# Kernel tuning notes

Measured on AMD Instinct MI355X. Metric: run time of the kernel, lower is better.

Reference implementation:

```python
import jax, jax.numpy as jnp
import numpy as np

NUM_PROJS = 7
BLOCK_SIZE = 256   # key block size
SAMPLE_SIZE = 256  # residual sampled keys


def _gray_perm(n):
    # AngularLSH._unit_hamming_distance_array: Gray-code bucket permutation
    a = np.array([0, 1], dtype=np.int32)
    for i in range(1, n):
        a = np.concatenate([a, a[::-1] + 2 ** i])
    return a

PERM = jnp.asarray(_gray_perm(NUM_PROJS))
ENC = jnp.asarray(2 ** np.arange(NUM_PROJS), dtype=jnp.int32)


def lsh_hash(x, proj_dir):
    # sign-bit angular LSH -> Gray-code bucket id, [B,H,N]
    bits = (jnp.einsum('bhnd,dr->bhnr', x, proj_dir) > 0).astype(jnp.int32)
    return PERM[(bits * ENC).sum(-1)]


def exact_attention(q, k, v, scale, bias=None):
    s = jnp.einsum('...qd,...kd->...qk', q, k) * scale
    if bias is not None:
        s = s + bias
    lse = jax.nn.logsumexp(s, axis=-1, keepdims=True)
    attn = jnp.einsum('...qk,...kd->...qd', jnp.exp(s - lse), v)
    return attn, lse


def add_self_attentions(a1, l1, a2, l2):
    # stable online-softmax combination of two attention partials
    c = jax.nn.sigmoid(l1 - l2)  # = exp(l1)/(exp(l1)+exp(l2))
    return c * a1 + (1.0 - c) * a2, jnp.logaddexp(l1, l2)


def gather_seq(x, idx):
    # x: [B,H,N,D], idx: [B,H,S] -> [B,H,S,D]
    return jnp.take_along_axis(x, idx[..., None], axis=2)


def hyper_attention(query, key, value, proj_dir, sampled_set):
    B, H, Nq, D = query.shape
    Nk = key.shape[2]
    scale = D ** -0.5
    # --- LSH bucket sort of queries and keys (stable, matches torch.sort stable=True) ---
    q_idx = jnp.argsort(lsh_hash(query, proj_dir), axis=2, stable=True)
    k_idx = jnp.argsort(lsh_hash(key, proj_dir), axis=2, stable=True)
    q_idx_inv = jnp.argsort(q_idx, axis=2, stable=True)
    q_s = gather_seq(query, q_idx)
    k_s = gather_seq(key, k_idx)
    v_s = gather_seq(value, k_idx)
    # --- block-diagonal attention over LSH-sorted blocks ---
    nb = Nk // BLOCK_SIZE          # 32 blocks
    qbs = Nq // nb                 # query block size (== 256 here)
    attn_b, lse_b = exact_attention(
        q_s.reshape(B, H, nb, qbs, D),
        k_s.reshape(B, H, nb, BLOCK_SIZE, D),
        v_s.reshape(B, H, nb, BLOCK_SIZE, D),
        scale)
    attn_b = attn_b.reshape(B, H, Nq, D)
    lse_b = lse_b.reshape(B, H, Nq, 1)
    # --- residual: uniformly sampled keys, importance weight Nk/SAMPLE_SIZE ---
    k_sub = gather_seq(k_s, sampled_set)
    v_sub = gather_seq(v_s, sampled_set)
    q_pos = jnp.arange(Nq) // qbs                    # [Nq] query block ids
    s_blk = sampled_set // BLOCK_SIZE                # [B,H,S] sampled key block ids
    overlap = q_pos[None, None, :, None] == s_blk[:, :, None, :]  # [B,H,Nq,S]
    bias = jnp.where(overlap, jnp.finfo(query.dtype).min, 0.0).astype(query.dtype)
    attn_r, lse_r = exact_attention(q_s, k_sub, v_sub, scale, bias)
    lse_r = lse_r + jnp.asarray(np.log(Nk / SAMPLE_SIZE), lse_r.dtype)
    # --- combine partials via online LSE, then unsort queries ---
    attn, lse = add_self_attentions(attn_b, lse_b, attn_r, lse_r)
    attn = gather_seq(attn, q_idx_inv)
    return attn


def setup_inputs() -> dict:
    key = jax.random.key(0)
    kq, kk, kv, kp, ks = jax.random.split(key, 5)
    B, H, N, D = 2, 16, 8192, 64
    return {
        'query': jax.random.normal(kq, (B, H, N, D), jnp.float32),
        'key': jax.random.normal(kk, (B, H, N, D), jnp.float32),
        'value': jax.random.normal(kv, (B, H, N, D), jnp.float32),
        'proj_dir': jax.random.normal(kp, (D, NUM_PROJS), jnp.float32),
        'sampled_set': jax.random.randint(ks, (B, H, SAMPLE_SIZE), 0, N),
    }


def reference(query, key, value, proj_dir, sampled_set):
    return hyper_attention(query, key, value, proj_dir, sampled_set)
```

## Files before the change

### kernel.cpp

```cpp
#include <hip/hip_runtime.h>

#define BHX   32
#define NSEQ  8192
#define NMASK 8191
#define DIM   64
#define NPROJ 7
#define NBUCK 128
#define NBLK  32
#define QBS   256
#define SSIZE 256
#define LOG32 3.4657359027997265f
#define KPAD  72

typedef unsigned short u16;
typedef unsigned int   u32;
typedef unsigned char  u8;
typedef __attribute__((ext_vector_type(8))) short bf16x8;
typedef __attribute__((ext_vector_type(4))) float f32x4;

union B8U { u32 u[4]; bf16x8 v; };

__device__ __forceinline__ u16 f2bf(float f){
    u32 u = __float_as_uint(f);
    u32 r = u + 0x7fffu + ((u >> 16) & 1u);
    return (u16)(r >> 16);
}
__device__ __forceinline__ u32 pk2(float a, float b){
    return (u32)f2bf(a) | ((u32)f2bf(b) << 16);
}
__device__ __forceinline__ f32x4 mfma16(bf16x8 a, bf16x8 b, f32x4 c){
    return __builtin_amdgcn_mfma_f32_16x16x32_bf16(a, b, c, 0, 0, 0);
}

__global__ __launch_bounds__(256) void hash_kernel(
    const float* __restrict__ qg, const float* __restrict__ kg,
    const float* __restrict__ projg,
    u8* __restrict__ bkt)
{
    const int slab = blockIdx.x, bh = blockIdx.y, tz = blockIdx.z;
    const float* __restrict__ x = tz ? kg : qg;
    u8* __restrict__ ob = bkt + ((size_t)tz * BHX + bh) * NSEQ;

    __shared__ float projs[NPROJ][DIM];
    const int t = threadIdx.x;
    if (t < 112) {
        #pragma unroll
        for (int u = 0; u < 4; u++) {
            int e = t * 4 + u;
            projs[e % NPROJ][e / NPROJ] = projg[e];
        }
    }
    __syncthreads();

    const size_t bhN = (size_t)bh * NSEQ;
    #pragma unroll
    for (int j = 0; j < 4; j++) {
        int n = slab * 1024 + j * 256 + t;
        const float4* row = (const float4*)(x + (bhN + n) * DIM);
        float dot[NPROJ];
        #pragma unroll
        for (int r = 0; r < NPROJ; r++) dot[r] = 0.0f;
        #pragma unroll
        for (int c = 0; c < 16; c++) {
            float4 w = row[c];
            float f[4] = {w.x, w.y, w.z, w.w};
            #pragma unroll
            for (int u = 0; u < 4; u++) {
                float xv = f[u];
                int d = c * 4 + u;
                #pragma unroll
                for (int r = 0; r < NPROJ; r++) dot[r] += xv * projs[r][d];
            }
        }
        int code = 0;
        #pragma unroll
        for (int r = 0; r < NPROJ; r++) code |= (dot[r] > 0.0f ? 1 : 0) << r;
        ob[n] = (u8)(code ^ (code >> 1));
    }
}

__global__ __launch_bounds__(256) void sort_kernel(
    const u8* __restrict__ bkt,
    u16* __restrict__ qidx, u16* __restrict__ kidx)
{
    const int bh = blockIdx.x, tz = blockIdx.y;
    const u8* __restrict__ ib = bkt + ((size_t)tz * BHX + bh) * NSEQ;
    u16* __restrict__ idx = (tz ? kidx : qidx) + (size_t)bh * NSEQ;

    __shared__ u8  lb[NSEQ];
    __shared__ u16 hist[NBUCK][258];
    __shared__ int base[NBUCK];
    __shared__ int tot[NBUCK];

    const int t = threadIdx.x;
    {
        const uint4* src = (const uint4*)ib;
        uint4* dst = (uint4*)lb;
        dst[t] = src[t];
        dst[256 + t] = src[256 + t];
    }
    u32* hz = (u32*)&hist[0][0];
    for (int z = t; z < (NBUCK * 258) / 2; z += 256) hz[z] = 0u;
    __syncthreads();

    #pragma unroll 4
    for (int i = 0; i < 32; i++) hist[lb[t * 32 + i]][t]++;
    __syncthreads();

    if (t < NBUCK) {
        u32 run = 0;
        for (int c = 0; c < 256; c++) {
            u32 v = hist[t][c];
            hist[t][c] = (u16)run;
            run += v;
        }
        tot[t] = (int)run;
    }
    __syncthreads();
    if (t == 0) {
        int run = 0;
        for (int b = 0; b < NBUCK; b++) { base[b] = run; run += tot[b]; }
    }
    __syncthreads();

    #pragma unroll 4
    for (int i = 0; i < 32; i++) {
        int n = t * 32 + i;
        int b = lb[n];
        int pos = base[b] + hist[b][t];
        hist[b][t]++;
        idx[pos] = (u16)n;
    }
}

__global__ __launch_bounds__(256, 2) void attn_mfma(
    const float* __restrict__ qg, const float* __restrict__ kg,
    const float* __restrict__ vg,
    const u16* __restrict__ qidx, const u16* __restrict__ kidx,
    const int* __restrict__ samp,
    float* __restrict__ outg)
{
    __shared__ u16  Ks[64 * KPAD];
    __shared__ u16  Vt[64 * KPAD];
    __shared__ u16  Ps[4 * 64 * KPAD];
    __shared__ float addv[64];

    const int qb = blockIdx.x, bh = blockIdx.y, t = threadIdx.x;
    const int w = t >> 6, lane = t & 63, c = lane & 15, g = lane >> 4;
    const size_t bhN = (size_t)bh * NSEQ;

    int qi[4];
    bf16x8 qf[4][2];
    #pragma unroll
    for (int qt = 0; qt < 4; qt++) {
        qi[qt] = ((int)qidx[bhN + qb * QBS + w * 64 + qt * 16 + c]) & NMASK;
        const float* qr = qg + (bhN + (size_t)qi[qt]) * DIM;
        #pragma unroll
        for (int dk = 0; dk < 2; dk++) {
            int d0 = dk * 32 + g * 8;
            float4 x = *(const float4*)(qr + d0);
            float4 y = *(const float4*)(qr + d0 + 4);
            B8U f;
            f.u[0] = pk2(x.x * 0.125f, x.y * 0.125f);
            f.u[1] = pk2(x.z * 0.125f, x.w * 0.125f);
            f.u[2] = pk2(y.x * 0.125f, y.y * 0.125f);
            f.u[3] = pk2(y.z * 0.125f, y.w * 0.125f);
            qf[qt][dk] = f.v;
        }
    }

    f32x4 O[4][4];
    #pragma unroll
    for (int dt = 0; dt < 4; dt++)
        #pragma unroll
        for (int qt = 0; qt < 4; qt++) O[dt][qt] = (f32x4)0.0f;
    float m[4] = {-1e30f, -1e30f, -1e30f, -1e30f};
    float l[4] = {0.0f, 0.0f, 0.0f, 0.0f};

    for (int cc = 0; cc < 8; cc++) {
        __syncthreads();
        {
            int s = t >> 2, seg = (t & 3) * 16;
            int grow; float add;
            if (cc < 4) {
                grow = ((int)kidx[bhN + qb * QBS + cc * 64 + s]) & NMASK;
                add  = 0.0f;
            } else {
                int sidx = samp[bh * SSIZE + (cc - 4) * 64 + s] & NMASK;
                grow = ((int)kidx[bhN + sidx]) & NMASK;
                add  = ((sidx >> 8) == qb) ? -1e30f : LOG32;
            }
            const float4* kr = (const float4*)(kg + (bhN + (size_t)grow) * DIM + seg);
            float4 a = kr[0], b = kr[1], e = kr[2], d = kr[3];
            u32* dst = (u32*)&Ks[s * KPAD + seg];
            dst[0] = pk2(a.x, a.y); dst[1] = pk2(a.z, a.w);
            dst[2] = pk2(b.x, b.y); dst[3] = pk2(b.z, b.w);
            dst[4] = pk2(e.x, e.y); dst[5] = pk2(e.z, e.w);
            dst[6] = pk2(d.x, d.y); dst[7] = pk2(d.z, d.w);
            const float4* vr = (const float4*)(vg + (bhN + (size_t)grow) * DIM + seg);
            float4 va = vr[0], vb = vr[1], vc = vr[2], vd = vr[3];
            float vv[16] = {va.x, va.y, va.z, va.w, vb.x, vb.y, vb.z, vb.w,
                            vc.x, vc.y, vc.z, vc.w, vd.x, vd.y, vd.z, vd.w};
            #pragma unroll
            for (int i = 0; i < 16; i++) Vt[(seg + i) * KPAD + s] = f2bf(vv[i]);
            if ((t & 3) == 0) addv[s] = add;
        }
        __syncthreads();

        f32x4 addn[4];
        #pragma unroll
        for (int kt = 0; kt < 4; kt++)
            addn[kt] = *(const f32x4*)&addv[kt * 16 + g * 4];

        bf16x8 ka[4][2];
        #pragma unroll
        for (int kt = 0; kt < 4; kt++)
            #pragma unroll
            for (int dk = 0; dk < 2; dk++)
                ka[kt][dk] = *(const bf16x8*)&Ks[(kt * 16 + c) * KPAD + dk * 32 + g * 8];

        #pragma unroll
        for (int qt = 0; qt < 4; qt++) {
            f32x4 S[4];
            #pragma unroll
            for (int kt = 0; kt < 4; kt++) {
                S[kt] = (f32x4)0.0f;
                S[kt] = mfma16(ka[kt][0], qf[qt][0], S[kt]);
                S[kt] = mfma16(ka[kt][1], qf[qt][1], S[kt]);
            }
            float cmax = -1e30f;
            #pragma unroll
            for (int kt = 0; kt < 4; kt++)
                #pragma unroll
                for (int r = 0; r < 4; r++)
                    cmax = fmaxf(cmax, S[kt][r] + addn[kt][r]);
            cmax = fmaxf(cmax, __shfl_xor(cmax, 16));
            cmax = fmaxf(cmax, __shfl_xor(cmax, 32));
            float mnew  = fmaxf(m[qt], cmax);
            float alpha = __expf(m[qt] - mnew);
            m[qt] = mnew;
            float lsum = 0.0f;
            u16* prow = &Ps[(size_t)(w * 64 + qt * 16 + c) * KPAD];
            #pragma unroll
            for (int kt = 0; kt < 4; kt++) {
                float p0 = __expf(S[kt][0] + addn[kt][0] - mnew);
                float p1 = __expf(S[kt][1] + addn[kt][1] - mnew);
                float p2 = __expf(S[kt][2] + addn[kt][2] - mnew);
                float p3 = __expf(S[kt][3] + addn[kt][3] - mnew);
                lsum += (p0 + p1) + (p2 + p3);
                u32* pw = (u32*)&prow[kt * 16 + g * 4];
                pw[0] = pk2(p0, p1);
                pw[1] = pk2(p2, p3);
            }
            lsum += __shfl_xor(lsum, 16);
            lsum += __shfl_xor(lsum, 32);
            l[qt] = l[qt] * alpha + lsum;
            #pragma unroll
            for (int dt = 0; dt < 4; dt++) O[dt][qt] *= alpha;
        }

        #pragma unroll
        for (int kk = 0; kk < 2; kk++) {
            bf16x8 vfr[4], pfr[4];
            #pragma unroll
            for (int dt = 0; dt < 4; dt++)
                vfr[dt] = *(const bf16x8*)&Vt[(dt * 16 + c) * KPAD + kk * 32 + g * 8];
            #pragma unroll
            for (int qt = 0; qt < 4; qt++)
                pfr[qt] = *(const bf16x8*)&Ps[(size_t)(w * 64 + qt * 16 + c) * KPAD + kk * 32 + g * 8];
            #pragma unroll
            for (int dt = 0; dt < 4; dt++)
                #pragma unroll
                for (int qt = 0; qt < 4; qt++)
                    O[dt][qt] = mfma16(vfr[dt], pfr[qt], O[dt][qt]);
        }
    }

    #pragma unroll
    for (int qt = 0; qt < 4; qt++) {
        float inv = 1.0f / fmaxf(l[qt], 1e-30f);
        float* orow = outg + (bhN + (size_t)qi[qt]) * DIM;
        #pragma unroll
        for (int dt = 0; dt < 4; dt++) {
            f32x4 o = O[dt][qt] * inv;
            *(f32x4*)(orow + dt * 16 + g * 4) = o;
        }
    }
}

extern "C" void kernel_launch(void* const* d_in, const int* in_sizes, int n_in,
                              void* d_out, int out_size, void* d_ws, size_t ws_size,
                              hipStream_t stream)
{
    const float* qg   = (const float*)d_in[0];
    const float* kg   = (const float*)d_in[1];
    const float* vg   = (const float*)d_in[2];
    const float* pg   = (const float*)d_in[3];
    const int*   samp = (const int*)d_in[4];
    float* outg = (float*)d_out;

    u16* qidx = (u16*)d_ws;
    u16* kidx = qidx + BHX * NSEQ;
    u8*  bkt  = (u8*)(kidx + BHX * NSEQ);

    hipLaunchKernelGGL(hash_kernel, dim3(8, BHX, 2), dim3(256), 0, stream,
                       qg, kg, pg, bkt);
    hipLaunchKernelGGL(sort_kernel, dim3(BHX, 2), dim3(256), 0, stream,
                       bkt, qidx, kidx);
    hipLaunchKernelGGL(attn_mfma, dim3(NBLK, BHX), dim3(256), 0, stream,
                       qg, kg, vg, qidx, kidx, samp, outg);
}
```

Before: 314.4 us.

## Use 512-thread attention blocks, split K/V staging, swizzle V transpose, vectorize hash

The attention kernel moves to 512 threads per block, with each wave owning 32 queries instead of 64. This lowers per-thread register use and raises the number of waves per CU. The K and V loads are split between the two halves of the block, and the transposed V tile uses an XOR swizzle to cut LDS bank conflicts. The additive mask is folded into S right after the MFMA. The hash kernel reads the projection vectors from LDS as float4. The risk is that the smaller per-wave work makes each V fragment reused across fewer query tiles.

```diff
diff --git a/kernel.cpp b/kernel.cpp
--- a/kernel.cpp
+++ b/kernel.cpp
@@ -62,14 +62,14 @@
         for (int r = 0; r < NPROJ; r++) dot[r] = 0.0f;
         #pragma unroll
         for (int c = 0; c < 16; c++) {
-            float4 w = row[c];
-            float f[4] = {w.x, w.y, w.z, w.w};
-            #pragma unroll
-            for (int u = 0; u < 4; u++) {
-                float xv = f[u];
-                int d = c * 4 + u;
-                #pragma unroll
-                for (int r = 0; r < NPROJ; r++) dot[r] += xv * projs[r][d];
+            float4 wv = row[c];
+            #pragma unroll
+            for (int r = 0; r < NPROJ; r++) {
+                float4 p = *(const float4*)&projs[r][c * 4];
+                dot[r] += wv.x * p.x;
+                dot[r] += wv.y * p.y;
+                dot[r] += wv.z * p.z;
+                dot[r] += wv.w * p.w;
             }
         }
         int code = 0;
@@ -133,7 +133,7 @@
     }
 }
 
-__global__ __launch_bounds__(256, 2) void attn_mfma(
+__global__ __launch_bounds__(512, 4) void attn_mfma(
     const float* __restrict__ qg, const float* __restrict__ kg,
     const float* __restrict__ vg,
     const u16* __restrict__ qidx, const u16* __restrict__ kidx,
@@ -142,45 +142,47 @@
 {
     __shared__ u16  Ks[64 * KPAD];
     __shared__ u16  Vt[64 * KPAD];
-    __shared__ u16  Ps[4 * 64 * KPAD];
+    __shared__ u16  Ps[256 * KPAD];
     __shared__ float addv[64];
 
     const int qb = blockIdx.x, bh = blockIdx.y, t = threadIdx.x;
     const int w = t >> 6, lane = t & 63, c = lane & 15, g = lane >> 4;
     const size_t bhN = (size_t)bh * NSEQ;
 
-    int qi[4];
-    bf16x8 qf[4][2];
+    int qi[2];
+    bf16x8 qf[2][2];
     #pragma unroll
-    for (int qt = 0; qt < 4; qt++) {
-        qi[qt] = ((int)qidx[bhN + qb * QBS + w * 64 + qt * 16 + c]) & NMASK;
+    for (int qt = 0; qt < 2; qt++) {
+        qi[qt] = ((int)qidx[bhN + qb * QBS + w * 32 + qt * 16 + c]) & NMASK;
         const float* qr = qg + (bhN + (size_t)qi[qt]) * DIM;
         #pragma unroll
         for (int dk = 0; dk < 2; dk++) {
             int d0 = dk * 32 + g * 8;
-            float4 x = *(const float4*)(qr + d0);
-            float4 y = *(const float4*)(qr + d0 + 4);
+            float4 xx = *(const float4*)(qr + d0);
+            float4 yy = *(const float4*)(qr + d0 + 4);
             B8U f;
-            f.u[0] = pk2(x.x * 0.125f, x.y * 0.125f);
-            f.u[1] = pk2(x.z * 0.125f, x.w * 0.125f);
-            f.u[2] = pk2(y.x * 0.125f, y.y * 0.125f);
-            f.u[3] = pk2(y.z * 0.125f, y.w * 0.125f);
+            f.u[0] = pk2(xx.x * 0.125f, xx.y * 0.125f);
+            f.u[1] = pk2(xx.z * 0.125f, xx.w * 0.125f);
+            f.u[2] = pk2(yy.x * 0.125f, yy.y * 0.125f);
+            f.u[3] = pk2(yy.z * 0.125f, yy.w * 0.125f);
             qf[qt][dk] = f.v;
         }
     }
 
-    f32x4 O[4][4];
+    f32x4 O[4][2];
     #pragma unroll
     for (int dt = 0; dt < 4; dt++)
         #pragma unroll
-        for (int qt = 0; qt < 4; qt++) O[dt][qt] = (f32x4)0.0f;
-    float m[4] = {-1e30f, -1e30f, -1e30f, -1e30f};
-    float l[4] = {0.0f, 0.0f, 0.0f, 0.0f};
+        for (int qt = 0; qt < 2; qt++) O[dt][qt] = (f32x4)0.0f;
+    float m[2] = {-1e30f, -1e30f};
+    float l[2] = {0.0f, 0.0f};
 
     for (int cc = 0; cc < 8; cc++) {
         __syncthreads();
         {
-            int s = t >> 2, seg = (t & 3) * 16;
+            const int half = t >> 8;
+            const int tt = t & 255;
+            const int s = tt >> 2, seg = (tt & 3) * 16;
             int grow; float add;
             if (cc < 4) {
                 grow = ((int)kidx[bhN + qb * QBS + cc * 64 + s]) & NMASK;
@@ -190,27 +192,27 @@
                 grow = ((int)kidx[bhN + sidx]) & NMASK;
                 add  = ((sidx >> 8) == qb) ? -1e30f : LOG32;
             }
-            const float4* kr = (const float4*)(kg + (bhN + (size_t)grow) * DIM + seg);
-            float4 a = kr[0], b = kr[1], e = kr[2], d = kr[3];
-            u32* dst = (u32*)&Ks[s * KPAD + seg];
-            dst[0] = pk2(a.x, a.y); dst[1] = pk2(a.z, a.w);
-            dst[2] = pk2(b.x, b.y); dst[3] = pk2(b.z, b.w);
-            dst[4] = pk2(e.x, e.y); dst[5] = pk2(e.z, e.w);
-            dst[6] = pk2(d.x, d.y); dst[7] = pk2(d.z, d.w);
-            const float4* vr = (const float4*)(vg + (bhN + (size_t)grow) * DIM + seg);
-            float4 va = vr[0], vb = vr[1], vc = vr[2], vd = vr[3];
-            float vv[16] = {va.x, va.y, va.z, va.w, vb.x, vb.y, vb.z, vb.w,
-                            vc.x, vc.y, vc.z, vc.w, vd.x, vd.y, vd.z, vd.w};
-            #pragma unroll
-            for (int i = 0; i < 16; i++) Vt[(seg + i) * KPAD + s] = f2bf(vv[i]);
-            if ((t & 3) == 0) addv[s] = add;
+            if (half == 0) {
+                const float4* kr = (const float4*)(kg + (bhN + (size_t)grow) * DIM + seg);
+                float4 a = kr[0], b = kr[1], e = kr[2], d = kr[3];
+                u32* dst = (u32*)&Ks[s * KPAD + seg];
+                dst[0] = pk2(a.x, a.y); dst[1] = pk2(a.z, a.w);
+                dst[2] = pk2(b.x, b.y); dst[3] = pk2(b.z, b.w);
+                dst[4] = pk2(e.x, e.y); dst[5] = pk2(e.z, e.w);
+                dst[6] = pk2(d.x, d.y); dst[7] = pk2(d.z, d.w);
+                if ((tt & 3) == 0) addv[s] = add;
+            } else {
+                const float4* vr = (const float4*)(vg + (bhN + (size_t)grow) * DIM + seg);
+                float4 va = vr[0], vb = vr[1], ve = vr[2], vd = vr[3];
+                float vv[16] = {va.x, va.y, va.z, va.w, vb.x, vb.y, vb.z, vb.w,
+                                ve.x, ve.y, ve.z, ve.w, vd.x, vd.y, vd.z, vd.w};
+                const int col = (((s >> 3) ^ (tt & 3)) << 3) | (s & 7);
+                #pragma unroll
+                for (int i = 0; i < 16; i++)
+                    Vt[(seg + i) * KPAD + col] = f2bf(vv[i]);
+            }
         }
         __syncthreads();
-
-        f32x4 addn[4];
-        #pragma unroll
-        for (int kt = 0; kt < 4; kt++)
-            addn[kt] = *(const f32x4*)&addv[kt * 16 + g * 4];
 
         bf16x8 ka[4][2];
         #pragma unroll
@@ -220,33 +222,34 @@
                 ka[kt][dk] = *(const bf16x8*)&Ks[(kt * 16 + c) * KPAD + dk * 32 + g * 8];
 
         #pragma unroll
-        for (int qt = 0; qt < 4; qt++) {
+        for (int qt = 0; qt < 2; qt++) {
             f32x4 S[4];
             #pragma unroll
             for (int kt = 0; kt < 4; kt++) {
                 S[kt] = (f32x4)0.0f;
                 S[kt] = mfma16(ka[kt][0], qf[qt][0], S[kt]);
                 S[kt] = mfma16(ka[kt][1], qf[qt][1], S[kt]);
+                S[kt] += *(const f32x4*)&addv[kt * 16 + g * 4];
             }
             float cmax = -1e30f;
             #pragma unroll
             for (int kt = 0; kt < 4; kt++)
                 #pragma unroll
                 for (int r = 0; r < 4; r++)
-                    cmax = fmaxf(cmax, S[kt][r] + addn[kt][r]);
+                    cmax = fmaxf(cmax, S[kt][r]);
             cmax = fmaxf(cmax, __shfl_xor(cmax, 16));
             cmax = fmaxf(cmax, __shfl_xor(cmax, 32));
             float mnew  = fmaxf(m[qt], cmax);
             float alpha = __expf(m[qt] - mnew);
             m[qt] = mnew;
             float lsum = 0.0f;
-            u16* prow = &Ps[(size_t)(w * 64 + qt * 16 + c) * KPAD];
+            u16* prow = &Ps[(size_t)(w * 32 + qt * 16 + c) * KPAD];
             #pragma unroll
             for (int kt = 0; kt < 4; kt++) {
-                float p0 = __expf(S[kt][0] + addn[kt][0] - mnew);
-                float p1 = __expf(S[kt][1] + addn[kt][1] - mnew);
-                float p2 = __expf(S[kt][2] + addn[kt][2] - mnew);
-                float p3 = __expf(S[kt][3] + addn[kt][3] - mnew);
+                float p0 = __expf(S[kt][0] - mnew);
+                float p1 = __expf(S[kt][1] - mnew);
+                float p2 = __expf(S[kt][2] - mnew);
+                float p3 = __expf(S[kt][3] - mnew);
                 lsum += (p0 + p1) + (p2 + p3);
                 u32* pw = (u32*)&prow[kt * 16 + g * 4];
                 pw[0] = pk2(p0, p1);
@@ -261,23 +264,24 @@
 
         #pragma unroll
         for (int kk = 0; kk < 2; kk++) {
-            bf16x8 vfr[4], pfr[4];
+            bf16x8 vfr[4];
             #pragma unroll
             for (int dt = 0; dt < 4; dt++)
-                vfr[dt] = *(const bf16x8*)&Vt[(dt * 16 + c) * KPAD + kk * 32 + g * 8];
-            #pragma unroll
-            for (int qt = 0; qt < 4; qt++)
-                pfr[qt] = *(const bf16x8*)&Ps[(size_t)(w * 64 + qt * 16 + c) * KPAD + kk * 32 + g * 8];
-            #pragma unroll
-            for (int dt = 0; dt < 4; dt++)
+                vfr[dt] = *(const bf16x8*)&Vt[(dt * 16 + c) * KPAD
+                                              + (((4 * kk + g) ^ dt) << 3)];
+            #pragma unroll
+            for (int qt = 0; qt < 2; qt++) {
+                bf16x8 pfr = *(const bf16x8*)&Ps[(size_t)(w * 32 + qt * 16 + c) * KPAD
+                                                 + kk * 32 + g * 8];
                 #pragma unroll
-                for (int qt = 0; qt < 4; qt++)
-                    O[dt][qt] = mfma16(vfr[dt], pfr[qt], O[dt][qt]);
+                for (int dt = 0; dt < 4; dt++)
+                    O[dt][qt] = mfma16(vfr[dt], pfr, O[dt][qt]);
+            }
         }
     }
 
     #pragma unroll
-    for (int qt = 0; qt < 4; qt++) {
+    for (int qt = 0; qt < 2; qt++) {
         float inv = 1.0f / fmaxf(l[qt], 1e-30f);
         float* orow = outg + (bhN + (size_t)qi[qt]) * DIM;
         #pragma unroll
@@ -307,6 +311,6 @@
                        qg, kg, pg, bkt);
     hipLaunchKernelGGL(sort_kernel, dim3(BHX, 2), dim3(256), 0, stream,
                        bkt, qidx, kidx);
-    hipLaunchKernelGGL(attn_mfma, dim3(NBLK, BHX), dim3(256), 0, stream,
+    hipLaunchKernelGGL(attn_mfma, dim3(NBLK, BHX), dim3(512), 0, stream,
                        qg, kg, vg, qidx, kidx, samp, outg);
 }
```

Measured after the change: 345.3 us. 1.1x slower.

## Keep softmax probabilities in registers via key permutation; use exp2 and parallel scans

Applied to the files above, without the earlier changes.

The attention kernel loads keys in a permuted row order (kp), so the MFMA score output layout lines up with the B-operand layout for the PV product. Probabilities can then be packed straight from registers instead of round-tripping through the Ps shared buffer. Queries are prescaled by scale*log2(e) so exp2 can replace expf, and the sampled-key bias becomes log2(32)=5. V is transposed by pairs of keys to write packed u32 stores, and V fragments are hoisted out of the query loop. In the sort kernel the histogram scan is vectorized as u16 pairs and the bucket base scan uses a wave shuffle; the hash kernel reads the projections as float4. The risks are correctness of the permutation mapping and higher register pressure.

```diff
diff --git a/kernel.cpp b/kernel.cpp
--- a/kernel.cpp
+++ b/kernel.cpp
@@ -9,8 +9,8 @@
 #define NBLK  32
 #define QBS   256
 #define SSIZE 256
-#define LOG32 3.4657359027997265f
 #define KPAD  72
+#define QSC   0.18033688f
 
 typedef unsigned short u16;
 typedef unsigned int   u32;
@@ -62,14 +62,14 @@
         for (int r = 0; r < NPROJ; r++) dot[r] = 0.0f;
         #pragma unroll
         for (int c = 0; c < 16; c++) {
-            float4 w = row[c];
-            float f[4] = {w.x, w.y, w.z, w.w};
-            #pragma unroll
-            for (int u = 0; u < 4; u++) {
-                float xv = f[u];
-                int d = c * 4 + u;
-                #pragma unroll
-                for (int r = 0; r < NPROJ; r++) dot[r] += xv * projs[r][d];
+            float4 wv = row[c];
+            #pragma unroll
+            for (int r = 0; r < NPROJ; r++) {
+                float4 p = *(const float4*)&projs[r][c * 4];
+                dot[r] += wv.x * p.x;
+                dot[r] += wv.y * p.y;
+                dot[r] += wv.z * p.z;
+                dot[r] += wv.w * p.w;
             }
         }
         int code = 0;
@@ -108,18 +108,30 @@
     __syncthreads();
 
     if (t < NBUCK) {
+        u32* hrow = (u32*)&hist[t][0];
         u32 run = 0;
-        for (int c = 0; c < 256; c++) {
-            u32 v = hist[t][c];
-            hist[t][c] = (u16)run;
-            run += v;
+        #pragma unroll 8
+        for (int c = 0; c < 128; c++) {
+            u32 v = hrow[c];
+            u32 lo = v & 0xffffu, hi = v >> 16;
+            hrow[c] = run | ((run + lo) << 16);
+            run += lo + hi;
         }
         tot[t] = (int)run;
     }
     __syncthreads();
-    if (t == 0) {
-        int run = 0;
-        for (int b = 0; b < NBUCK; b++) { base[b] = run; run += tot[b]; }
+
+    if (t < 64) {
+        int a = tot[2 * t], b = tot[2 * t + 1];
+        int s = a + b;
+        #pragma unroll
+        for (int d = 1; d < 64; d <<= 1) {
+            int v = __shfl_up(s, d);
+            if (t >= d) s += v;
+        }
+        int excl = s - (a + b);
+        base[2 * t]     = excl;
+        base[2 * t + 1] = excl + a;
     }
     __syncthreads();
 
@@ -142,7 +154,6 @@
 {
     __shared__ u16  Ks[64 * KPAD];
     __shared__ u16  Vt[64 * KPAD];
-    __shared__ u16  Ps[4 * 64 * KPAD];
     __shared__ float addv[64];
 
     const int qb = blockIdx.x, bh = blockIdx.y, t = threadIdx.x;
@@ -158,13 +169,13 @@
         #pragma unroll
         for (int dk = 0; dk < 2; dk++) {
             int d0 = dk * 32 + g * 8;
-            float4 x = *(const float4*)(qr + d0);
-            float4 y = *(const float4*)(qr + d0 + 4);
+            float4 xx = *(const float4*)(qr + d0);
+            float4 yy = *(const float4*)(qr + d0 + 4);
             B8U f;
-            f.u[0] = pk2(x.x * 0.125f, x.y * 0.125f);
-            f.u[1] = pk2(x.z * 0.125f, x.w * 0.125f);
-            f.u[2] = pk2(y.x * 0.125f, y.y * 0.125f);
-            f.u[3] = pk2(y.z * 0.125f, y.w * 0.125f);
+            f.u[0] = pk2(xx.x * QSC, xx.y * QSC);
+            f.u[1] = pk2(xx.z * QSC, xx.w * QSC);
+            f.u[2] = pk2(yy.x * QSC, yy.y * QSC);
+            f.u[3] = pk2(yy.z * QSC, yy.w * QSC);
             qf[qt][dk] = f.v;
         }
     }
@@ -177,33 +188,54 @@
     float m[4] = {-1e30f, -1e30f, -1e30f, -1e30f};
     float l[4] = {0.0f, 0.0f, 0.0f, 0.0f};
 
+    const int ks_row = t >> 2, ks_q = t & 3;
+    const int kp = ((ks_row >> 5) << 5) | (((ks_row >> 2) & 3) << 3)
+                 | (((ks_row >> 4) & 1) << 2) | (ks_row & 3);
+    const int vs_p = t & 31, vs_seg = (t >> 5) * 8;
+
+    #pragma unroll 1
     for (int cc = 0; cc < 8; cc++) {
         __syncthreads();
         {
-            int s = t >> 2, seg = (t & 3) * 16;
             int grow; float add;
             if (cc < 4) {
-                grow = ((int)kidx[bhN + qb * QBS + cc * 64 + s]) & NMASK;
+                grow = ((int)kidx[bhN + qb * QBS + cc * 64 + kp]) & NMASK;
                 add  = 0.0f;
             } else {
-                int sidx = samp[bh * SSIZE + (cc - 4) * 64 + s] & NMASK;
+                int sidx = samp[bh * SSIZE + (cc - 4) * 64 + kp] & NMASK;
                 grow = ((int)kidx[bhN + sidx]) & NMASK;
-                add  = ((sidx >> 8) == qb) ? -1e30f : LOG32;
-            }
-            const float4* kr = (const float4*)(kg + (bhN + (size_t)grow) * DIM + seg);
-            float4 a = kr[0], b = kr[1], e = kr[2], d = kr[3];
-            u32* dst = (u32*)&Ks[s * KPAD + seg];
-            dst[0] = pk2(a.x, a.y); dst[1] = pk2(a.z, a.w);
-            dst[2] = pk2(b.x, b.y); dst[3] = pk2(b.z, b.w);
-            dst[4] = pk2(e.x, e.y); dst[5] = pk2(e.z, e.w);
-            dst[6] = pk2(d.x, d.y); dst[7] = pk2(d.z, d.w);
-            const float4* vr = (const float4*)(vg + (bhN + (size_t)grow) * DIM + seg);
-            float4 va = vr[0], vb = vr[1], vc = vr[2], vd = vr[3];
-            float vv[16] = {va.x, va.y, va.z, va.w, vb.x, vb.y, vb.z, vb.w,
-                            vc.x, vc.y, vc.z, vc.w, vd.x, vd.y, vd.z, vd.w};
-            #pragma unroll
-            for (int i = 0; i < 16; i++) Vt[(seg + i) * KPAD + s] = f2bf(vv[i]);
-            if ((t & 3) == 0) addv[s] = add;
+                add  = ((sidx >> 8) == qb) ? -1e30f : 5.0f;
+            }
+            const float4* kr = (const float4*)(kg + (bhN + (size_t)grow) * DIM + ks_q * 16);
+            float4 ak = kr[0], bk = kr[1], ck = kr[2], ek = kr[3];
+            u32* dst = (u32*)&Ks[ks_row * KPAD + ks_q * 16];
+            dst[0] = pk2(ak.x, ak.y); dst[1] = pk2(ak.z, ak.w);
+            dst[2] = pk2(bk.x, bk.y); dst[3] = pk2(bk.z, bk.w);
+            dst[4] = pk2(ck.x, ck.y); dst[5] = pk2(ck.z, ck.w);
+            dst[6] = pk2(ek.x, ek.y); dst[7] = pk2(ek.z, ek.w);
+            if (ks_q == 0) addv[ks_row] = add;
+
+            int n0 = 2 * vs_p, n1 = n0 + 1;
+            int g0, g1;
+            if (cc < 4) {
+                g0 = ((int)kidx[bhN + qb * QBS + cc * 64 + n0]) & NMASK;
+                g1 = ((int)kidx[bhN + qb * QBS + cc * 64 + n1]) & NMASK;
+            } else {
+                int s0 = samp[bh * SSIZE + (cc - 4) * 64 + n0] & NMASK;
+                int s1 = samp[bh * SSIZE + (cc - 4) * 64 + n1] & NMASK;
+                g0 = ((int)kidx[bhN + s0]) & NMASK;
+                g1 = ((int)kidx[bhN + s1]) & NMASK;
+            }
+            const float4* v0 = (const float4*)(vg + (bhN + (size_t)g0) * DIM + vs_seg);
+            const float4* v1 = (const float4*)(vg + (bhN + (size_t)g1) * DIM + vs_seg);
+            float4 a0 = v0[0], b0 = v0[1];
+            float4 a1 = v1[0], b1 = v1[1];
+            float va[8] = {a0.x, a0.y, a0.z, a0.w, b0.x, b0.y, b0.z, b0.w};
+            float vb[8] = {a1.x, a1.y, a1.z, a1.w, b1.x, b1.y, b1.z, b1.w};
+            u32* vtu = (u32*)Vt;
+            #pragma unroll
+            for (int i = 0; i < 8; i++)
+                vtu[(vs_seg + i) * (KPAD / 2) + vs_p] = pk2(va[i], vb[i]);
         }
         __syncthreads();
 
@@ -216,8 +248,15 @@
         #pragma unroll
         for (int kt = 0; kt < 4; kt++)
             #pragma unroll
-            for (int dk = 0; dk < 2; dk++)
-                ka[kt][dk] = *(const bf16x8*)&Ks[(kt * 16 + c) * KPAD + dk * 32 + g * 8];
+            for (int dd = 0; dd < 2; dd++)
+                ka[kt][dd] = *(const bf16x8*)&Ks[(kt * 16 + c) * KPAD + dd * 32 + g * 8];
+
+        bf16x8 vfr[2][4];
+        #pragma unroll
+        for (int kk = 0; kk < 2; kk++)
+            #pragma unroll
+            for (int dt = 0; dt < 4; dt++)
+                vfr[kk][dt] = *(const bf16x8*)&Vt[(dt * 16 + c) * KPAD + kk * 32 + g * 8];
 
         #pragma unroll
         for (int qt = 0; qt < 4; qt++) {
@@ -227,52 +266,48 @@
                 S[kt] = (f32x4)0.0f;
                 S[kt] = mfma16(ka[kt][0], qf[qt][0], S[kt]);
                 S[kt] = mfma16(ka[kt][1], qf[qt][1], S[kt]);
+                S[kt] += addn[kt];
             }
             float cmax = -1e30f;
             #pragma unroll
             for (int kt = 0; kt < 4; kt++)
                 #pragma unroll
                 for (int r = 0; r < 4; r++)
-                    cmax = fmaxf(cmax, S[kt][r] + addn[kt][r]);
+                    cmax = fmaxf(cmax, S[kt][r]);
             cmax = fmaxf(cmax, __shfl_xor(cmax, 16));
             cmax = fmaxf(cmax, __shfl_xor(cmax, 32));
             float mnew  = fmaxf(m[qt], cmax);
-            float alpha = __expf(m[qt] - mnew);
+            float alpha = __builtin_exp2f(m[qt] - mnew);
             m[qt] = mnew;
             float lsum = 0.0f;
-            u16* prow = &Ps[(size_t)(w * 64 + qt * 16 + c) * KPAD];
+            u32 pp[4][2];
             #pragma unroll
             for (int kt = 0; kt < 4; kt++) {
-                float p0 = __expf(S[kt][0] + addn[kt][0] - mnew);
-                float p1 = __expf(S[kt][1] + addn[kt][1] - mnew);
-                float p2 = __expf(S[kt][2] + addn[kt][2] - mnew);
-                float p3 = __expf(S[kt][3] + addn[kt][3] - mnew);
+                float p0 = __builtin_exp2f(S[kt][0] - mnew);
+                float p1 = __builtin_exp2f(S[kt][1] - mnew);
+                float p2 = __builtin_exp2f(S[kt][2] - mnew);
+                float p3 = __builtin_exp2f(S[kt][3] - mnew);
                 lsum += (p0 + p1) + (p2 + p3);
-                u32* pw = (u32*)&prow[kt * 16 + g * 4];
-                pw[0] = pk2(p0, p1);
-                pw[1] = pk2(p2, p3);
+                pp[kt][0] = pk2(p0, p1);
+                pp[kt][1] = pk2(p2, p3);
             }
             lsum += __shfl_xor(lsum, 16);
             lsum += __shfl_xor(lsum, 32);
             l[qt] = l[qt] * alpha + lsum;
             #pragma unroll
             for (int dt = 0; dt < 4; dt++) O[dt][qt] *= alpha;
-        }
-
-        #pragma unroll
-        for (int kk = 0; kk < 2; kk++) {
-            bf16x8 vfr[4], pfr[4];
-            #pragma unroll
-            for (int dt = 0; dt < 4; dt++)
-                vfr[dt] = *(const bf16x8*)&Vt[(dt * 16 + c) * KPAD + kk * 32 + g * 8];
-            #pragma unroll
-            for (int qt = 0; qt < 4; qt++)
-                pfr[qt] = *(const bf16x8*)&Ps[(size_t)(w * 64 + qt * 16 + c) * KPAD + kk * 32 + g * 8];
-            #pragma unroll
-            for (int dt = 0; dt < 4; dt++)
+
+            #pragma unroll
+            for (int kk = 0; kk < 2; kk++) {
+                B8U pf;
+                pf.u[0] = pp[2 * kk][0];
+                pf.u[1] = pp[2 * kk][1];
+                pf.u[2] = pp[2 * kk + 1][0];
+                pf.u[3] = pp[2 * kk + 1][1];
                 #pragma unroll
-                for (int qt = 0; qt < 4; qt++)
-                    O[dt][qt] = mfma16(vfr[dt], pfr[qt], O[dt][qt]);
+                for (int dt = 0; dt < 4; dt++)
+                    O[dt][qt] = mfma16(vfr[kk][dt], pf.v, O[dt][qt]);
+            }
         }
     }
 
```

Result: slower. 337.2 us (+7.3%).
